# Performance work log

Measured on AMD Instinct MI355X. Metric: run time of the kernel, lower is better.

## Reference

```python
import jax, jax.numpy as jnp
import numpy as np

N = 100000   # nodes
E = 3200000  # directed edges
F_IN = 128   # data.num_node_features
H = 16       # hidden
C = 2        # output classes (hard-coded in module)


def _glorot(key, fan_in, fan_out):
    s = jnp.sqrt(6.0 / (fan_in + fan_out)).astype(jnp.float32)
    return jax.random.uniform(key, (fan_in, fan_out), jnp.float32, -s, s)


def setup_inputs() -> dict:
    key = jax.random.key(0)
    ks = jax.random.split(key, 5)
    x = jax.random.normal(ks[0], (N, F_IN), jnp.float32)
    edge_index = jax.random.randint(ks[1], (2, E), 0, N, dtype=jnp.int64)
    return {
        "x": x,
        "edge_index": edge_index,
        "W1": _glorot(ks[2], F_IN, H), "b1": jnp.zeros((H,), jnp.float32),
        "W2": _glorot(ks[3], H, H),    "b2": jnp.zeros((H,), jnp.float32),
        "W3": _glorot(ks[4], H, C),    "b3": jnp.zeros((C,), jnp.float32),
    }


def _gcn_conv(x, W, b, src, dst, norm, n):
    # PyG GCNConv: linear transform, then normalized gather -> scatter-add, + bias
    h = x @ W                                   # [N, out]
    msg = h[src] * norm[:, None]                # [E+N, out] gather over source nodes
    out = jax.ops.segment_sum(msg, dst, num_segments=n)  # scatter-add at targets
    return out + b


def reference(x, edge_index, W1, b1, W2, b2, W3, b3):
    n = x.shape[0]
    loop = jnp.arange(n, dtype=edge_index.dtype)
    src = jnp.concatenate([edge_index[0], loop])  # add self-loops (PyG default)
    dst = jnp.concatenate([edge_index[1], loop])
    # symmetric normalization: deg^{-1/2}[src] * deg^{-1/2}[dst], deg = in-degree w/ self-loops
    deg = jax.ops.segment_sum(jnp.ones(src.shape, jnp.float32), dst, num_segments=n)
    dis = jnp.where(deg > 0, jax.lax.rsqrt(jnp.maximum(deg, 1.0)), 0.0)
    norm = dis[src] * dis[dst]
    # dropout is identity in eval mode
    h = jax.nn.relu(_gcn_conv(x, W1, b1, src, dst, norm, n))
    h = jax.nn.relu(_gcn_conv(h, W2, b2, src, dst, norm, n))
    h = _gcn_conv(h, W3, b3, src, dst, norm, n)
    return jax.nn.log_softmax(h, axis=1)
```

## Files before the change

### kernel.cpp

```cpp
#include <hip/hip_runtime.h>
#include <math.h>

#define NSB  512
#define BSH  9
#define BKN  512
#define ESMAX 6272
#define TPB  8

typedef _Float16 h8  __attribute__((ext_vector_type(8)));
typedef _Float16 h2v __attribute__((ext_vector_type(2)));


__global__ void k_scan1(const int* __restrict__ in, int* __restrict__ out,
                        int* __restrict__ bsum, int n) {
    __shared__ int sd[256];
    int base = blockIdx.x * 2048 + threadIdx.x * 8;
    int v[8];
    int ts = 0;
#pragma unroll
    for (int j = 0; j < 8; j++) {
        int idx = base + j;
        v[j] = ts;
        ts += (idx < n) ? in[idx] : 0;
    }
    sd[threadIdx.x] = ts;
    __syncthreads();
    for (int ofs = 1; ofs < 256; ofs <<= 1) {
        int t = (threadIdx.x >= (unsigned)ofs) ? sd[threadIdx.x - ofs] : 0;
        __syncthreads();
        sd[threadIdx.x] += t;
        __syncthreads();
    }
    int excl = (threadIdx.x == 0) ? 0 : sd[threadIdx.x - 1];
#pragma unroll
    for (int j = 0; j < 8; j++) {
        int idx = base + j;
        if (idx < n) out[idx] = excl + v[j];
    }
    if (threadIdx.x == 255) bsum[blockIdx.x] = sd[255];
}

__global__ void k_scan2(int* __restrict__ bsum, int nb) {
    __shared__ int sd[256];
    int orig = (threadIdx.x < (unsigned)nb) ? bsum[threadIdx.x] : 0;
    sd[threadIdx.x] = orig;
    __syncthreads();
    for (int ofs = 1; ofs < 256; ofs <<= 1) {
        int t = (threadIdx.x >= (unsigned)ofs) ? sd[threadIdx.x - ofs] : 0;
        __syncthreads();
        sd[threadIdx.x] += t;
        __syncthreads();
    }
    if (threadIdx.x < (unsigned)nb) bsum[threadIdx.x] = sd[threadIdx.x] - orig;
}

__global__ void k_scan3(int* __restrict__ out, const int* __restrict__ bsum, int n) {
    int i = blockIdx.x * blockDim.x + threadIdx.x;
    if (i < n) out[i] += bsum[i >> 11];
}


__global__ void k_hist(const int* __restrict__ dst, int* __restrict__ hist,
                       int e, int nbuck, int es) {
    __shared__ int h[256];
    for (int i = threadIdx.x; i < 256; i += blockDim.x) h[i] = 0;
    __syncthreads();
    int lo = blockIdx.x * es;
    int hi = min(lo + es, e);
    for (int i = lo + threadIdx.x; i < hi; i += blockDim.x)
        atomicAdd(&h[dst[i] >> BSH], 1);
    __syncthreads();
    for (int i = threadIdx.x; i < nbuck; i += blockDim.x)
        hist[(size_t)i * gridDim.x + blockIdx.x] = h[i];
}

__global__ void k_bucket(const int* __restrict__ src, const int* __restrict__ dst,
                         const int* __restrict__ offs, unsigned* __restrict__ col,
                         int e, int nbuck, int es) {
    __shared__ unsigned sorted[ESMAX];
    __shared__ unsigned char sbuck[ESMAX];
    __shared__ int lc[256], lsc[256], lofE[256], lcur[256], soff[256];
    int tid = threadIdx.x;
    lc[tid] = 0;
    if (tid < nbuck) soff[tid] = offs[(size_t)tid * gridDim.x + blockIdx.x];
    __syncthreads();
    int lo = blockIdx.x * es;
    int hi = min(lo + es, e);
    for (int i = lo + tid; i < hi; i += 256)
        atomicAdd(&lc[dst[i] >> BSH], 1);
    __syncthreads();
    lsc[tid] = lc[tid];
    __syncthreads();
    for (int ofs = 1; ofs < 256; ofs <<= 1) {
        int t = (tid >= ofs) ? lsc[tid - ofs] : 0;
        __syncthreads();
        lsc[tid] += t;
        __syncthreads();
    }
    int excl = (tid == 0) ? 0 : lsc[tid - 1];
    lofE[tid] = excl;
    lcur[tid] = excl;
    __syncthreads();
    for (int i = lo + tid; i < hi; i += 256) {
        int d = dst[i];
        int b = d >> BSH;
        int p = atomicAdd(&lcur[b], 1);
        sorted[p] = ((unsigned)src[i] << BSH) | (unsigned)(d & (BKN - 1));
        sbuck[p] = (unsigned char)b;
    }
    __syncthreads();
    int cnt = hi - lo;
    for (int i = tid; i < cnt; i += 256) {
        int b = sbuck[i];
        col[soff[b] + (i - lofE[b])] = sorted[i];
    }
}

__global__ void k_sort(const unsigned* __restrict__ col, const int* __restrict__ offs,
                       int* __restrict__ col2, int* __restrict__ rs,
                       float* __restrict__ dis, int n, int e, int nbuck) {
    __shared__ int cnt[BKN];
    __shared__ int sd[BKN];
    __shared__ int cur[BKN];
    int tid = threadIdx.x;
    int b = blockIdx.x;
    int lo = offs[(size_t)b * NSB];
    int hi = (b + 1 < nbuck) ? offs[(size_t)(b + 1) * NSB] : e;
    if (tid < BKN) cnt[tid] = 0;
    __syncthreads();
    for (int i = lo + tid; i < hi; i += 1024)
        atomicAdd(&cnt[col[i] & (BKN - 1u)], 1);
    __syncthreads();
    if (tid < BKN) sd[tid] = cnt[tid];
    __syncthreads();
    for (int ofs = 1; ofs < BKN; ofs <<= 1) {
        int t = (tid < BKN && tid >= ofs) ? sd[tid - ofs] : 0;
        __syncthreads();
        if (tid < BKN) sd[tid] += t;
        __syncthreads();
    }
    if (tid < BKN) {
        int excl = (tid == 0) ? 0 : sd[tid - 1];
        cur[tid] = lo + excl;
        int node = (b << BSH) + tid;
        if (node < n) {
            rs[node] = lo + excl;
            dis[node] = rsqrtf((float)(cnt[tid] + 1));
        }
    }
    if (b == 0 && tid == 0) rs[n] = e;
    __syncthreads();
    for (int i = lo + tid; i < hi; i += 1024) {
        unsigned v = col[i];
        int pos = atomicAdd(&cur[v & (BKN - 1u)], 1);
        col2[pos] = (int)(v >> BSH);
    }
}


__global__ void k_linear1s(const float* __restrict__ x, const float* __restrict__ W,
                           const float* __restrict__ dis, _Float16* __restrict__ hs,
                           int n, int ntiles) {
    __shared__ float sWT[16 * 132];
    __shared__ float sx[16 * 132];
    int tid = threadIdx.x;
    for (int i = tid; i < 2048; i += 256) {
        int k = i >> 4, c = i & 15;
        sWT[c * 132 + k] = W[i];
    }
    int tile0 = blockIdx.x * TPB;
    const float4* xg4 = (const float4*)x;
    for (int tile = tile0; tile < tile0 + TPB && tile < ntiles; tile++) {
        int nodeBase = tile * 16;
        __syncthreads();
        for (int i = tid; i < 512; i += 256) {
            int nl = i >> 5, k4 = i & 31;
            int nd = nodeBase + nl;
            float4 v = make_float4(0.f, 0.f, 0.f, 0.f);
            if (nd < n) v = xg4[(size_t)nd * 32 + k4];
            *((float4*)(sx + nl * 132 + k4 * 4)) = v;
        }
        __syncthreads();
        int nl = tid >> 4, c = tid & 15;
        int node = nodeBase + nl;
        const float4* xr = (const float4*)(sx + nl * 132);
        const float4* wr = (const float4*)(sWT + c * 132);
        float acc = 0.f;
#pragma unroll
        for (int k4 = 0; k4 < 32; k4++) {
            float4 xv = xr[k4];
            float4 wv = wr[k4];
            acc += xv.x * wv.x + xv.y * wv.y + xv.z * wv.z + xv.w * wv.w;
        }
        if (node < n)
            hs[(size_t)node * 16 + c] = (_Float16)(acc * dis[node]);
    }
}


__global__ void k_pullA(const _Float16* __restrict__ hs, const int* __restrict__ rs,
                        const int* __restrict__ col2, const float* __restrict__ dis,
                        const float* __restrict__ bb, const float* __restrict__ W,
                        _Float16* __restrict__ hsOut, int n) {
    __shared__ float sW[256];
    __shared__ float sb[16];
    if (threadIdx.x < 256) sW[threadIdx.x] = W[threadIdx.x];
    if (threadIdx.x < 16) sb[threadIdx.x] = bb[threadIdx.x];
    __syncthreads();
    int t = blockIdx.x * blockDim.x + threadIdx.x;
    int node = t >> 1, q = t & 1;
    if (node >= n) return;
    const h8* H = (const h8*)hs;
    h8 self = H[(size_t)node * 2 + q];
    float acc[8];
#pragma unroll
    for (int j = 0; j < 8; j++) acc[j] = (float)self[j];
    int b = rs[node], e2 = rs[node + 1];
    int i = b;
    for (; i + 3 < e2; i += 4) {
        int s0 = col2[i], s1 = col2[i + 1], s2 = col2[i + 2], s3 = col2[i + 3];
        h8 v0 = H[(size_t)s0 * 2 + q];
        h8 v1 = H[(size_t)s1 * 2 + q];
        h8 v2 = H[(size_t)s2 * 2 + q];
        h8 v3 = H[(size_t)s3 * 2 + q];
#pragma unroll
        for (int j = 0; j < 8; j++)
            acc[j] += (float)v0[j] + (float)v1[j] + (float)v2[j] + (float)v3[j];
    }
    for (; i < e2; i++) {
        h8 v = H[(size_t)col2[i] * 2 + q];
#pragma unroll
        for (int j = 0; j < 8; j++) acc[j] += (float)v[j];
    }
    float d = dis[node];
    float va[16];
#pragma unroll
    for (int j = 0; j < 8; j++) {
        int k = q * 8 + j;
        float v = acc[j] * d + sb[k];
        v = v > 0.f ? v : 0.f;
        float other = __shfl_xor(v, 1);
        va[j]     = q ? other : v;
        va[8 + j] = q ? v : other;
    }
    h8 o;
#pragma unroll
    for (int j = 0; j < 8; j++) {
        int c = q * 8 + j;
        float s = 0.f;
#pragma unroll
        for (int k = 0; k < 16; k++) s += va[k] * sW[k * 16 + c];
        o[j] = (_Float16)(s * d);
    }
    ((h8*)hsOut)[(size_t)node * 2 + q] = o;
}


__global__ void k_pullB(const _Float16* __restrict__ hs, const int* __restrict__ rs,
                        const int* __restrict__ col2, const float* __restrict__ dis,
                        const float* __restrict__ bb, const float* __restrict__ W,
                        _Float16* __restrict__ hs2, int n) {
    __shared__ float sW[32];
    __shared__ float sb[16];
    if (threadIdx.x < 32) sW[threadIdx.x] = W[threadIdx.x];
    if (threadIdx.x < 16) sb[threadIdx.x] = bb[threadIdx.x];
    __syncthreads();
    int t = blockIdx.x * blockDim.x + threadIdx.x;
    int node = t >> 1, q = t & 1;
    if (node >= n) return;
    const h8* H = (const h8*)hs;
    h8 self = H[(size_t)node * 2 + q];
    float acc[8];
#pragma unroll
    for (int j = 0; j < 8; j++) acc[j] = (float)self[j];
    int b = rs[node], e2 = rs[node + 1];
    int i = b;
    for (; i + 3 < e2; i += 4) {
        int s0 = col2[i], s1 = col2[i + 1], s2 = col2[i + 2], s3 = col2[i + 3];
        h8 v0 = H[(size_t)s0 * 2 + q];
        h8 v1 = H[(size_t)s1 * 2 + q];
        h8 v2 = H[(size_t)s2 * 2 + q];
        h8 v3 = H[(size_t)s3 * 2 + q];
#pragma unroll
        for (int j = 0; j < 8; j++)
            acc[j] += (float)v0[j] + (float)v1[j] + (float)v2[j] + (float)v3[j];
    }
    for (; i < e2; i++) {
        h8 v = H[(size_t)col2[i] * 2 + q];
#pragma unroll
        for (int j = 0; j < 8; j++) acc[j] += (float)v[j];
    }
    float d = dis[node];
    float p0 = 0.f, p1 = 0.f;
#pragma unroll
    for (int j = 0; j < 8; j++) {
        int k = q * 8 + j;
        float v = acc[j] * d + sb[k];
        v = v > 0.f ? v : 0.f;
        p0 += v * sW[k * 2 + 0];
        p1 += v * sW[k * 2 + 1];
    }
    p0 += __shfl_xor(p0, 1);
    p1 += __shfl_xor(p1, 1);
    if (q == 0) {
        h2v o;
        o[0] = (_Float16)(p0 * d);
        o[1] = (_Float16)(p1 * d);
        ((h2v*)hs2)[node] = o;
    }
}


__global__ void k_pull2lsm(const _Float16* __restrict__ hs2, const int* __restrict__ rs,
                           const int* __restrict__ col2, const float* __restrict__ dis,
                           const float* __restrict__ b3, float* __restrict__ out, int n) {
    int node = blockIdx.x * blockDim.x + threadIdx.x;
    if (node >= n) return;
    const h2v* H = (const h2v*)hs2;
    h2v self = H[node];
    float a0 = (float)self[0], a1 = (float)self[1];
    int b = rs[node], e2 = rs[node + 1];
    int i = b;
    for (; i + 3 < e2; i += 4) {
        h2v v0 = H[col2[i]];
        h2v v1 = H[col2[i + 1]];
        h2v v2 = H[col2[i + 2]];
        h2v v3 = H[col2[i + 3]];
        a0 += (float)v0[0] + (float)v1[0] + (float)v2[0] + (float)v3[0];
        a1 += (float)v0[1] + (float)v1[1] + (float)v2[1] + (float)v3[1];
    }
    for (; i < e2; i++) {
        h2v v = H[col2[i]];
        a0 += (float)v[0];
        a1 += (float)v[1];
    }
    float d = dis[node];
    float z0 = a0 * d + b3[0];
    float z1 = a1 * d + b3[1];
    float m = fmaxf(z0, z1);
    float l = m + logf(expf(z0 - m) + expf(z1 - m));
    float2 o = {z0 - l, z1 - l};
    ((float2*)out)[node] = o;
}


extern "C" void kernel_launch(void* const* d_in, const int* in_sizes, int n_in,
                              void* d_out, int out_size, void* d_ws, size_t ws_size,
                              hipStream_t stream) {
    const float* x  = (const float*)d_in[0];
    const int*   ei = (const int*)d_in[1];
    const float* W1 = (const float*)d_in[2];
    const float* b1 = (const float*)d_in[3];
    const float* W2 = (const float*)d_in[4];
    const float* b2 = (const float*)d_in[5];
    const float* W3 = (const float*)d_in[6];
    const float* b3 = (const float*)d_in[7];
    float* out = (float*)d_out;

    const int N = in_sizes[0] / 128;
    const int E = in_sizes[1] / 2;
    const int* src = ei;
    const int* dst = ei + E;

    const int NBUCK = (N + BKN - 1) >> BSH;
    const int M = NBUCK * NSB;
    const int ES = (E + NSB - 1) / NSB;

    char* ws = (char*)d_ws;
    size_t off = 0;
    auto alloc = [&](size_t bytes) {
        void* p = ws + off;
        off += (bytes + 255) & ~(size_t)255;
        return p;
    };
    int*       hist = (int*)alloc((size_t)M * sizeof(int));
    int*       offs = (int*)alloc((size_t)M * sizeof(int));
    int*       bsum = (int*)alloc(256 * sizeof(int));
    unsigned*  col  = (unsigned*)alloc((size_t)E * sizeof(unsigned));
    int*       col2 = (int*)alloc((size_t)E * sizeof(int));
    int*       rs   = (int*)alloc((size_t)(N + 1) * sizeof(int));
    float*     dis  = (float*)alloc((size_t)N * sizeof(float));
    _Float16*  hsA  = (_Float16*)alloc((size_t)N * 16 * sizeof(_Float16));
    _Float16*  hsB  = (_Float16*)alloc((size_t)N * 16 * sizeof(_Float16));
    _Float16*  hs2  = (_Float16*)alloc((size_t)N * 2 * sizeof(_Float16));

    const int B = 256;
    auto g = [&](long long work) { return (int)((work + B - 1) / B); };
    const int NBS = (M + 2047) / 2048;

    k_hist<<<NSB, B, 0, stream>>>(dst, hist, E, NBUCK, ES);
    k_scan1<<<NBS, 256, 0, stream>>>(hist, offs, bsum, M);
    k_scan2<<<1, 256, 0, stream>>>(bsum, NBS);
    k_scan3<<<g(M), B, 0, stream>>>(offs, bsum, M);
    k_bucket<<<NSB, B, 0, stream>>>(src, dst, offs, col, E, NBUCK, ES);
    k_sort<<<NBUCK, 1024, 0, stream>>>(col, offs, col2, rs, dis, N, E, NBUCK);

    const int NTILES = (N + 15) / 16;
    k_linear1s<<<(NTILES + TPB - 1) / TPB, B, 0, stream>>>(x, W1, dis, hsA, N, NTILES);

    k_pullA<<<g((long long)N * 2), B, 0, stream>>>(hsA, rs, col2, dis, b1, W2, hsB, N);

    k_pullB<<<g((long long)N * 2), B, 0, stream>>>(hsB, rs, col2, dis, b2, W3, hs2, N);

    k_pull2lsm<<<g(N), B, 0, stream>>>(hs2, rs, col2, dis, b3, out, N);
}
```

Baseline: 281.4 us.

## Fuse CSR build kernels into one cooperative kernel with grid syncs

```diff
diff --git a/kernel.cpp b/kernel.cpp
--- a/kernel.cpp
+++ b/kernel.cpp
@@ -1,107 +1,99 @@
 #include <hip/hip_runtime.h>
+#include <hip/hip_cooperative_groups.h>
 #include <math.h>
 
-#define NSB  512
-#define BSH  9
-#define BKN  512
+namespace cg = cooperative_groups;
+
+#define NSB   512
+#define BTH   512
+#define BSH   9
+#define BKN   512
 #define ESMAX 6272
-#define TPB  8
+#define TPB   8
 
 typedef _Float16 h8  __attribute__((ext_vector_type(8)));
 typedef _Float16 h2v __attribute__((ext_vector_type(2)));
 
 
-__global__ void k_scan1(const int* __restrict__ in, int* __restrict__ out,
-                        int* __restrict__ bsum, int n) {
-    __shared__ int sd[256];
-    int base = blockIdx.x * 2048 + threadIdx.x * 8;
-    int v[8];
-    int ts = 0;
-#pragma unroll
-    for (int j = 0; j < 8; j++) {
-        int idx = base + j;
-        v[j] = ts;
-        ts += (idx < n) ? in[idx] : 0;
-    }
-    sd[threadIdx.x] = ts;
-    __syncthreads();
-    for (int ofs = 1; ofs < 256; ofs <<= 1) {
-        int t = (threadIdx.x >= (unsigned)ofs) ? sd[threadIdx.x - ofs] : 0;
-        __syncthreads();
-        sd[threadIdx.x] += t;
-        __syncthreads();
-    }
-    int excl = (threadIdx.x == 0) ? 0 : sd[threadIdx.x - 1];
-#pragma unroll
-    for (int j = 0; j < 8; j++) {
-        int idx = base + j;
-        if (idx < n) out[idx] = excl + v[j];
-    }
-    if (threadIdx.x == 255) bsum[blockIdx.x] = sd[255];
-}
-
-__global__ void k_scan2(int* __restrict__ bsum, int nb) {
-    __shared__ int sd[256];
-    int orig = (threadIdx.x < (unsigned)nb) ? bsum[threadIdx.x] : 0;
-    sd[threadIdx.x] = orig;
-    __syncthreads();
-    for (int ofs = 1; ofs < 256; ofs <<= 1) {
-        int t = (threadIdx.x >= (unsigned)ofs) ? sd[threadIdx.x - ofs] : 0;
-        __syncthreads();
-        sd[threadIdx.x] += t;
-        __syncthreads();
-    }
-    if (threadIdx.x < (unsigned)nb) bsum[threadIdx.x] = sd[threadIdx.x] - orig;
-}
-
-__global__ void k_scan3(int* __restrict__ out, const int* __restrict__ bsum, int n) {
-    int i = blockIdx.x * blockDim.x + threadIdx.x;
-    if (i < n) out[i] += bsum[i >> 11];
-}
-
-
-__global__ void k_hist(const int* __restrict__ dst, int* __restrict__ hist,
-                       int e, int nbuck, int es) {
-    __shared__ int h[256];
-    for (int i = threadIdx.x; i < 256; i += blockDim.x) h[i] = 0;
-    __syncthreads();
-    int lo = blockIdx.x * es;
-    int hi = min(lo + es, e);
-    for (int i = lo + threadIdx.x; i < hi; i += blockDim.x)
-        atomicAdd(&h[dst[i] >> BSH], 1);
-    __syncthreads();
-    for (int i = threadIdx.x; i < nbuck; i += blockDim.x)
-        hist[(size_t)i * gridDim.x + blockIdx.x] = h[i];
-}
-
-__global__ void k_bucket(const int* __restrict__ src, const int* __restrict__ dst,
-                         const int* __restrict__ offs, unsigned* __restrict__ col,
-                         int e, int nbuck, int es) {
+__global__ void k_build(const int* __restrict__ src, const int* __restrict__ dst,
+                        int* __restrict__ hist, int* __restrict__ bsum,
+                        unsigned* __restrict__ col, int* __restrict__ col2,
+                        int* __restrict__ rs, float* __restrict__ dis,
+                        int n, int e, int nbuck) {
+    cg::grid_group grid = cg::this_grid();
+    __shared__ int lc[512], lsc[512], lofE[512], lcur[512], soff[512];
     __shared__ unsigned sorted[ESMAX];
     __shared__ unsigned char sbuck[ESMAX];
-    __shared__ int lc[256], lsc[256], lofE[256], lcur[256], soff[256];
+
     int tid = threadIdx.x;
+    int blk = blockIdx.x;
+    int es = (e + NSB - 1) / NSB;
+    int lo = blk * es, hi = min(lo + es, e);
+
     lc[tid] = 0;
-    if (tid < nbuck) soff[tid] = offs[(size_t)tid * gridDim.x + blockIdx.x];
-    __syncthreads();
-    int lo = blockIdx.x * es;
-    int hi = min(lo + es, e);
-    for (int i = lo + tid; i < hi; i += 256)
+    __syncthreads();
+    for (int i = lo + tid; i < hi; i += BTH)
         atomicAdd(&lc[dst[i] >> BSH], 1);
     __syncthreads();
+    for (int i = tid; i < nbuck; i += BTH)
+        hist[(size_t)i * NSB + blk] = lc[i];
+    grid.sync();
+
+    const int M = nbuck * NSB;
+    const int seg = (M + NSB - 1) / NSB;
+    int sbase = blk * seg;
+    int v = 0;
+    bool inseg = (tid < seg) && (sbase + tid < M);
+    if (inseg) v = hist[sbase + tid];
+    lsc[tid] = v;
+    __syncthreads();
+    for (int ofs = 1; ofs < BTH; ofs <<= 1) {
+        int t = (tid >= ofs) ? lsc[tid - ofs] : 0;
+        __syncthreads();
+        lsc[tid] += t;
+        __syncthreads();
+    }
+    int excl = (tid == 0) ? 0 : lsc[tid - 1];
+    if (inseg) hist[sbase + tid] = excl;
+    if (tid == BTH - 1) bsum[blk] = lsc[BTH - 1];
+    grid.sync();
+
+    if (blk == 0) {
+        int b0 = bsum[tid];
+        lsc[tid] = b0;
+        __syncthreads();
+        for (int ofs = 1; ofs < BTH; ofs <<= 1) {
+            int t = (tid >= ofs) ? lsc[tid - ofs] : 0;
+            __syncthreads();
+            lsc[tid] += t;
+            __syncthreads();
+        }
+        bsum[tid] = lsc[tid] - b0;
+    }
+    grid.sync();
+
+    if (inseg) hist[sbase + tid] += bsum[blk];
+    grid.sync();
+
+    lc[tid] = 0;
+    if (tid < nbuck) soff[tid] = hist[(size_t)tid * NSB + blk];
+    __syncthreads();
+    for (int i = lo + tid; i < hi; i += BTH)
+        atomicAdd(&lc[dst[i] >> BSH], 1);
+    __syncthreads();
     lsc[tid] = lc[tid];
     __syncthreads();
-    for (int ofs = 1; ofs < 256; ofs <<= 1) {
+    for (int ofs = 1; ofs < BTH; ofs <<= 1) {
         int t = (tid >= ofs) ? lsc[tid - ofs] : 0;
         __syncthreads();
         lsc[tid] += t;
         __syncthreads();
     }
-    int excl = (tid == 0) ? 0 : lsc[tid - 1];
-    lofE[tid] = excl;
-    lcur[tid] = excl;
-    __syncthreads();
-    for (int i = lo + tid; i < hi; i += 256) {
+    int ex2 = (tid == 0) ? 0 : lsc[tid - 1];
+    lofE[tid] = ex2;
+    lcur[tid] = ex2;
+    __syncthreads();
+    for (int i = lo + tid; i < hi; i += BTH) {
         int d = dst[i];
         int b = d >> BSH;
         int p = atomicAdd(&lcur[b], 1);
@@ -109,51 +101,43 @@
         sbuck[p] = (unsigned char)b;
     }
     __syncthreads();
-    int cnt = hi - lo;
-    for (int i = tid; i < cnt; i += 256) {
+    int cnt_ = hi - lo;
+    for (int i = tid; i < cnt_; i += BTH) {
         int b = sbuck[i];
         col[soff[b] + (i - lofE[b])] = sorted[i];
     }
-}
-
-__global__ void k_sort(const unsigned* __restrict__ col, const int* __restrict__ offs,
-                       int* __restrict__ col2, int* __restrict__ rs,
-                       float* __restrict__ dis, int n, int e, int nbuck) {
-    __shared__ int cnt[BKN];
-    __shared__ int sd[BKN];
-    __shared__ int cur[BKN];
-    int tid = threadIdx.x;
-    int b = blockIdx.x;
-    int lo = offs[(size_t)b * NSB];
-    int hi = (b + 1 < nbuck) ? offs[(size_t)(b + 1) * NSB] : e;
-    if (tid < BKN) cnt[tid] = 0;
-    __syncthreads();
-    for (int i = lo + tid; i < hi; i += 1024)
-        atomicAdd(&cnt[col[i] & (BKN - 1u)], 1);
-    __syncthreads();
-    if (tid < BKN) sd[tid] = cnt[tid];
-    __syncthreads();
-    for (int ofs = 1; ofs < BKN; ofs <<= 1) {
-        int t = (tid < BKN && tid >= ofs) ? sd[tid - ofs] : 0;
-        __syncthreads();
-        if (tid < BKN) sd[tid] += t;
-        __syncthreads();
-    }
-    if (tid < BKN) {
-        int excl = (tid == 0) ? 0 : sd[tid - 1];
-        cur[tid] = lo + excl;
-        int node = (b << BSH) + tid;
+    grid.sync();
+
+    if (blk < nbuck) {
+        int blo = hist[(size_t)blk * NSB];
+        int bhi = (blk + 1 < nbuck) ? hist[(size_t)(blk + 1) * NSB] : e;
+        lc[tid] = 0;
+        __syncthreads();
+        for (int i = blo + tid; i < bhi; i += BTH)
+            atomicAdd(&lc[col[i] & (BKN - 1u)], 1);
+        __syncthreads();
+        lsc[tid] = lc[tid];
+        __syncthreads();
+        for (int ofs = 1; ofs < BTH; ofs <<= 1) {
+            int t = (tid >= ofs) ? lsc[tid - ofs] : 0;
+            __syncthreads();
+            lsc[tid] += t;
+            __syncthreads();
+        }
+        int ex3 = (tid == 0) ? 0 : lsc[tid - 1];
+        lcur[tid] = blo + ex3;
+        int node = (blk << BSH) + tid;
         if (node < n) {
-            rs[node] = lo + excl;
-            dis[node] = rsqrtf((float)(cnt[tid] + 1));
-        }
-    }
-    if (b == 0 && tid == 0) rs[n] = e;
-    __syncthreads();
-    for (int i = lo + tid; i < hi; i += 1024) {
-        unsigned v = col[i];
-        int pos = atomicAdd(&cur[v & (BKN - 1u)], 1);
-        col2[pos] = (int)(v >> BSH);
+            rs[node] = blo + ex3;
+            dis[node] = rsqrtf((float)(lc[tid] + 1));
+        }
+        if (blk == 0 && tid == 0) rs[n] = e;
+        __syncthreads();
+        for (int i = blo + tid; i < bhi; i += BTH) {
+            unsigned v2 = col[i];
+            int pos = atomicAdd(&lcur[v2 & (BKN - 1u)], 1);
+            col2[pos] = (int)(v2 >> BSH);
+        }
     }
 }
 
@@ -364,7 +348,6 @@
 
     const int NBUCK = (N + BKN - 1) >> BSH;
     const int M = NBUCK * NSB;
-    const int ES = (E + NSB - 1) / NSB;
 
     char* ws = (char*)d_ws;
     size_t off = 0;
@@ -374,8 +357,7 @@
         return p;
     };
     int*       hist = (int*)alloc((size_t)M * sizeof(int));
-    int*       offs = (int*)alloc((size_t)M * sizeof(int));
-    int*       bsum = (int*)alloc(256 * sizeof(int));
+    int*       bsum = (int*)alloc(NSB * sizeof(int));
     unsigned*  col  = (unsigned*)alloc((size_t)E * sizeof(unsigned));
     int*       col2 = (int*)alloc((size_t)E * sizeof(int));
     int*       rs   = (int*)alloc((size_t)(N + 1) * sizeof(int));
@@ -386,14 +368,17 @@
 
     const int B = 256;
     auto g = [&](long long work) { return (int)((work + B - 1) / B); };
-    const int NBS = (M + 2047) / 2048;
-
-    k_hist<<<NSB, B, 0, stream>>>(dst, hist, E, NBUCK, ES);
-    k_scan1<<<NBS, 256, 0, stream>>>(hist, offs, bsum, M);
-    k_scan2<<<1, 256, 0, stream>>>(bsum, NBS);
-    k_scan3<<<g(M), B, 0, stream>>>(offs, bsum, M);
-    k_bucket<<<NSB, B, 0, stream>>>(src, dst, offs, col, E, NBUCK, ES);
-    k_sort<<<NBUCK, 1024, 0, stream>>>(col, offs, col2, rs, dis, N, E, NBUCK);
+
+    {
+        int n_ = N, e_ = E, nb_ = NBUCK;
+        const int* src_ = src; const int* dst_ = dst;
+        int* hist_ = hist; int* bsum_ = bsum; unsigned* col_ = col;
+        int* col2_ = col2; int* rs_ = rs; float* dis_ = dis;
+        void* args[] = { &src_, &dst_, &hist_, &bsum_, &col_, &col2_,
+                         &rs_, &dis_, &n_, &e_, &nb_ };
+        hipLaunchCooperativeKernel((const void*)k_build, dim3(NSB), dim3(BTH),
+                                   args, 0, stream);
+    }
 
     const int NTILES = (N + 15) / 16;
     k_linear1s<<<(NTILES + TPB - 1) / TPB, B, 0, stream>>>(x, W1, dis, hsA, N, NTILES);
```

After: 561.6 us. 2x slower.

## Split neighbor lists across two threads and use finer dst buckets

Applied to the files above, without the earlier changes.

```diff
diff --git a/kernel.cpp b/kernel.cpp
--- a/kernel.cpp
+++ b/kernel.cpp
@@ -1,11 +1,11 @@
 #include <hip/hip_runtime.h>
 #include <math.h>
 
-#define NSB  512
-#define BSH  9
-#define BKN  512
+#define NSB   512
+#define BSH   8
+#define BKN   256
 #define ESMAX 6272
-#define TPB  8
+#define TPB   8
 
 typedef _Float16 h8  __attribute__((ext_vector_type(8)));
 typedef _Float16 h2v __attribute__((ext_vector_type(2)));
@@ -62,8 +62,8 @@
 
 __global__ void k_hist(const int* __restrict__ dst, int* __restrict__ hist,
                        int e, int nbuck, int es) {
-    __shared__ int h[256];
-    for (int i = threadIdx.x; i < 256; i += blockDim.x) h[i] = 0;
+    __shared__ int h[512];
+    for (int i = threadIdx.x; i < 512; i += blockDim.x) h[i] = 0;
     __syncthreads();
     int lo = blockIdx.x * es;
     int hi = min(lo + es, e);
@@ -79,19 +79,19 @@
                          int e, int nbuck, int es) {
     __shared__ unsigned sorted[ESMAX];
     __shared__ unsigned char sbuck[ESMAX];
-    __shared__ int lc[256], lsc[256], lofE[256], lcur[256], soff[256];
+    __shared__ int lc[512], lsc[512], lofE[512], lcur[512], soff[512];
     int tid = threadIdx.x;
     lc[tid] = 0;
     if (tid < nbuck) soff[tid] = offs[(size_t)tid * gridDim.x + blockIdx.x];
     __syncthreads();
     int lo = blockIdx.x * es;
     int hi = min(lo + es, e);
-    for (int i = lo + tid; i < hi; i += 256)
+    for (int i = lo + tid; i < hi; i += 512)
         atomicAdd(&lc[dst[i] >> BSH], 1);
     __syncthreads();
     lsc[tid] = lc[tid];
     __syncthreads();
-    for (int ofs = 1; ofs < 256; ofs <<= 1) {
+    for (int ofs = 1; ofs < 512; ofs <<= 1) {
         int t = (tid >= ofs) ? lsc[tid - ofs] : 0;
         __syncthreads();
         lsc[tid] += t;
@@ -101,17 +101,18 @@
     lofE[tid] = excl;
     lcur[tid] = excl;
     __syncthreads();
-    for (int i = lo + tid; i < hi; i += 256) {
+    for (int i = lo + tid; i < hi; i += 512) {
         int d = dst[i];
         int b = d >> BSH;
         int p = atomicAdd(&lcur[b], 1);
         sorted[p] = ((unsigned)src[i] << BSH) | (unsigned)(d & (BKN - 1));
-        sbuck[p] = (unsigned char)b;
-    }
-    __syncthreads();
-    int cnt = hi - lo;
-    for (int i = tid; i < cnt; i += 256) {
-        int b = sbuck[i];
+        sbuck[p] = (unsigned char)(b & 255);
+    }
+    __syncthreads();
+    int cnt_ = hi - lo;
+    int split = (nbuck > 256) ? lofE[256] : 0x7fffffff;
+    for (int i = tid; i < cnt_; i += 512) {
+        int b = sbuck[i] | ((i >= split) ? 256 : 0);
         col[soff[b] + (i - lofE[b])] = sorted[i];
     }
 }
@@ -128,7 +129,7 @@
     int hi = (b + 1 < nbuck) ? offs[(size_t)(b + 1) * NSB] : e;
     if (tid < BKN) cnt[tid] = 0;
     __syncthreads();
-    for (int i = lo + tid; i < hi; i += 1024)
+    for (int i = lo + tid; i < hi; i += 512)
         atomicAdd(&cnt[col[i] & (BKN - 1u)], 1);
     __syncthreads();
     if (tid < BKN) sd[tid] = cnt[tid];
@@ -150,7 +151,7 @@
     }
     if (b == 0 && tid == 0) rs[n] = e;
     __syncthreads();
-    for (int i = lo + tid; i < hi; i += 1024) {
+    for (int i = lo + tid; i < hi; i += 512) {
         unsigned v = col[i];
         int pos = atomicAdd(&cur[v & (BKN - 1u)], 1);
         col2[pos] = (int)(v >> BSH);
@@ -208,16 +209,24 @@
     if (threadIdx.x < 16) sb[threadIdx.x] = bb[threadIdx.x];
     __syncthreads();
     int t = blockIdx.x * blockDim.x + threadIdx.x;
-    int node = t >> 1, q = t & 1;
+    int node = t >> 2, sub = t & 3;
+    int q = sub & 1, half = sub >> 1;
     if (node >= n) return;
     const h8* H = (const h8*)hs;
-    h8 self = H[(size_t)node * 2 + q];
     float acc[8];
-#pragma unroll
-    for (int j = 0; j < 8; j++) acc[j] = (float)self[j];
+    if (half == 0) {
+        h8 self = H[(size_t)node * 2 + q];
+#pragma unroll
+        for (int j = 0; j < 8; j++) acc[j] = (float)self[j];
+    } else {
+#pragma unroll
+        for (int j = 0; j < 8; j++) acc[j] = 0.f;
+    }
     int b = rs[node], e2 = rs[node + 1];
-    int i = b;
-    for (; i + 3 < e2; i += 4) {
+    int mid = b + ((e2 - b) >> 1);
+    int i  = half ? mid : b;
+    int en = half ? e2  : mid;
+    for (; i + 3 < en; i += 4) {
         int s0 = col2[i], s1 = col2[i + 1], s2 = col2[i + 2], s3 = col2[i + 3];
         h8 v0 = H[(size_t)s0 * 2 + q];
         h8 v1 = H[(size_t)s1 * 2 + q];
@@ -227,11 +236,13 @@
         for (int j = 0; j < 8; j++)
             acc[j] += (float)v0[j] + (float)v1[j] + (float)v2[j] + (float)v3[j];
     }
-    for (; i < e2; i++) {
+    for (; i < en; i++) {
         h8 v = H[(size_t)col2[i] * 2 + q];
 #pragma unroll
         for (int j = 0; j < 8; j++) acc[j] += (float)v[j];
     }
+#pragma unroll
+    for (int j = 0; j < 8; j++) acc[j] += __shfl_xor(acc[j], 2);
     float d = dis[node];
     float va[16];
 #pragma unroll
@@ -243,16 +254,18 @@
         va[j]     = q ? other : v;
         va[8 + j] = q ? v : other;
     }
-    h8 o;
-#pragma unroll
-    for (int j = 0; j < 8; j++) {
-        int c = q * 8 + j;
-        float s = 0.f;
-#pragma unroll
-        for (int k = 0; k < 16; k++) s += va[k] * sW[k * 16 + c];
-        o[j] = (_Float16)(s * d);
-    }
-    ((h8*)hsOut)[(size_t)node * 2 + q] = o;
+    if (half == 0) {
+        h8 o;
+#pragma unroll
+        for (int j = 0; j < 8; j++) {
+            int c = q * 8 + j;
+            float s = 0.f;
+#pragma unroll
+            for (int k = 0; k < 16; k++) s += va[k] * sW[k * 16 + c];
+            o[j] = (_Float16)(s * d);
+        }
+        ((h8*)hsOut)[(size_t)node * 2 + q] = o;
+    }
 }
 
 
@@ -266,16 +279,24 @@
     if (threadIdx.x < 16) sb[threadIdx.x] = bb[threadIdx.x];
     __syncthreads();
     int t = blockIdx.x * blockDim.x + threadIdx.x;
-    int node = t >> 1, q = t & 1;
+    int node = t >> 2, sub = t & 3;
+    int q = sub & 1, half = sub >> 1;
     if (node >= n) return;
     const h8* H = (const h8*)hs;
-    h8 self = H[(size_t)node * 2 + q];
     float acc[8];
-#pragma unroll
-    for (int j = 0; j < 8; j++) acc[j] = (float)self[j];
+    if (half == 0) {
+        h8 self = H[(size_t)node * 2 + q];
+#pragma unroll
+        for (int j = 0; j < 8; j++) acc[j] = (float)self[j];
+    } else {
+#pragma unroll
+        for (int j = 0; j < 8; j++) acc[j] = 0.f;
+    }
     int b = rs[node], e2 = rs[node + 1];
-    int i = b;
-    for (; i + 3 < e2; i += 4) {
+    int mid = b + ((e2 - b) >> 1);
+    int i  = half ? mid : b;
+    int en = half ? e2  : mid;
+    for (; i + 3 < en; i += 4) {
         int s0 = col2[i], s1 = col2[i + 1], s2 = col2[i + 2], s3 = col2[i + 3];
         h8 v0 = H[(size_t)s0 * 2 + q];
         h8 v1 = H[(size_t)s1 * 2 + q];
@@ -285,11 +306,13 @@
         for (int j = 0; j < 8; j++)
             acc[j] += (float)v0[j] + (float)v1[j] + (float)v2[j] + (float)v3[j];
     }
-    for (; i < e2; i++) {
+    for (; i < en; i++) {
         h8 v = H[(size_t)col2[i] * 2 + q];
 #pragma unroll
         for (int j = 0; j < 8; j++) acc[j] += (float)v[j];
     }
+#pragma unroll
+    for (int j = 0; j < 8; j++) acc[j] += __shfl_xor(acc[j], 2);
     float d = dis[node];
     float p0 = 0.f, p1 = 0.f;
 #pragma unroll
@@ -302,7 +325,7 @@
     }
     p0 += __shfl_xor(p0, 1);
     p1 += __shfl_xor(p1, 1);
-    if (q == 0) {
+    if (sub == 0) {
         h2v o;
         o[0] = (_Float16)(p0 * d);
         o[1] = (_Float16)(p1 * d);
@@ -314,14 +337,20 @@
 __global__ void k_pull2lsm(const _Float16* __restrict__ hs2, const int* __restrict__ rs,
                            const int* __restrict__ col2, const float* __restrict__ dis,
                            const float* __restrict__ b3, float* __restrict__ out, int n) {
-    int node = blockIdx.x * blockDim.x + threadIdx.x;
+    int t = blockIdx.x * blockDim.x + threadIdx.x;
+    int node = t >> 1, half = t & 1;
     if (node >= n) return;
     const h2v* H = (const h2v*)hs2;
-    h2v self = H[node];
-    float a0 = (float)self[0], a1 = (float)self[1];
+    float a0 = 0.f, a1 = 0.f;
+    if (half == 0) {
+        h2v self = H[node];
+        a0 = (float)self[0]; a1 = (float)self[1];
+    }
     int b = rs[node], e2 = rs[node + 1];
-    int i = b;
-    for (; i + 3 < e2; i += 4) {
+    int mid = b + ((e2 - b) >> 1);
+    int i  = half ? mid : b;
+    int en = half ? e2  : mid;
+    for (; i + 3 < en; i += 4) {
         h2v v0 = H[col2[i]];
         h2v v1 = H[col2[i + 1]];
         h2v v2 = H[col2[i + 2]];
@@ -329,18 +358,22 @@
         a0 += (float)v0[0] + (float)v1[0] + (float)v2[0] + (float)v3[0];
         a1 += (float)v0[1] + (float)v1[1] + (float)v2[1] + (float)v3[1];
     }
-    for (; i < e2; i++) {
+    for (; i < en; i++) {
         h2v v = H[col2[i]];
         a0 += (float)v[0];
         a1 += (float)v[1];
     }
-    float d = dis[node];
-    float z0 = a0 * d + b3[0];
-    float z1 = a1 * d + b3[1];
-    float m = fmaxf(z0, z1);
-    float l = m + logf(expf(z0 - m) + expf(z1 - m));
-    float2 o = {z0 - l, z1 - l};
-    ((float2*)out)[node] = o;
+    a0 += __shfl_xor(a0, 1);
+    a1 += __shfl_xor(a1, 1);
+    if (half == 0) {
+        float d = dis[node];
+        float z0 = a0 * d + b3[0];
+        float z1 = a1 * d + b3[1];
+        float m = fmaxf(z0, z1);
+        float l = m + logf(expf(z0 - m) + expf(z1 - m));
+        float2 o = {z0 - l, z1 - l};
+        ((float2*)out)[node] = o;
+    }
 }
 
 
@@ -392,15 +425,15 @@
     k_scan1<<<NBS, 256, 0, stream>>>(hist, offs, bsum, M);
     k_scan2<<<1, 256, 0, stream>>>(bsum, NBS);
     k_scan3<<<g(M), B, 0, stream>>>(offs, bsum, M);
-    k_bucket<<<NSB, B, 0, stream>>>(src, dst, offs, col, E, NBUCK, ES);
-    k_sort<<<NBUCK, 1024, 0, stream>>>(col, offs, col2, rs, dis, N, E, NBUCK);
+    k_bucket<<<NSB, 512, 0, stream>>>(src, dst, offs, col, E, NBUCK, ES);
+    k_sort<<<NBUCK, 512, 0, stream>>>(col, offs, col2, rs, dis, N, E, NBUCK);
 
     const int NTILES = (N + 15) / 16;
     k_linear1s<<<(NTILES + TPB - 1) / TPB, B, 0, stream>>>(x, W1, dis, hsA, N, NTILES);
 
-    k_pullA<<<g((long long)N * 2), B, 0, stream>>>(hsA, rs, col2, dis, b1, W2, hsB, N);
-
-    k_pullB<<<g((long long)N * 2), B, 0, stream>>>(hsB, rs, col2, dis, b2, W3, hs2, N);
-
-    k_pull2lsm<<<g(N), B, 0, stream>>>(hs2, rs, col2, dis, b3, out, N);
-}
+    k_pullA<<<g((long long)N * 4), B, 0, stream>>>(hsA, rs, col2, dis, b1, W2, hsB, N);
+
+    k_pullB<<<g((long long)N * 4), B, 0, stream>>>(hsB, rs, col2, dis, b2, W3, hs2, N);
+
+    k_pull2lsm<<<g((long long)N * 2), B, 0, stream>>>(hs2, rs, col2, dis, b3, out, N);
+}
```

New measurement: 257.1 us. 1.09x faster.
